# Performance work log

Hardware: AMD Instinct MI355X
Metric: run time of the kernel (lower is better)

## Reference

```python
import jax, jax.numpy as jnp
import numpy as np

NUM_BITS = 8
EPS = 1e-8
N_HEADS = 16

def fake_quantize(t):
    # per-tensor symmetric fake quantization, matching fake_quantize_tensor
    qmax = 2 ** (NUM_BITS - 1) - 1
    qmin = -(2 ** (NUM_BITS - 1))
    max_abs = jnp.max(jnp.abs(jax.lax.stop_gradient(t)))
    scale = jnp.maximum(max_abs / qmax, EPS)
    q = jnp.clip(jnp.round(t / scale), qmin, qmax)
    return q * scale

def fq_linear(x, W, b):
    # F.linear(fake_quant(x), fake_quant(W), b)
    return fake_quantize(x) @ fake_quantize(W).T + b

def setup_inputs() -> dict:
    key = jax.random.key(0)
    ks = jax.random.split(key, 9)
    B, T, D = 2, 2048, 1024
    s = 0.02
    return {
        "x": jax.random.normal(ks[0], (B, T, D), jnp.float32),
        "Wq": jax.random.normal(ks[1], (D, D), jnp.float32) * s,
        "bq": jax.random.normal(ks[2], (D,), jnp.float32) * s,
        "Wk": jax.random.normal(ks[3], (D, D), jnp.float32) * s,
        "bk": jax.random.normal(ks[4], (D,), jnp.float32) * s,
        "Wv": jax.random.normal(ks[5], (D, D), jnp.float32) * s,
        "bv": jax.random.normal(ks[6], (D,), jnp.float32) * s,
        "Wo": jax.random.normal(ks[7], (D, D), jnp.float32) * s,
        "bo": jax.random.normal(ks[8], (D,), jnp.float32) * s,
    }

def reference(x, Wq, bq, Wk, bk, Wv, bv, Wo, bo):
    B, T, D = x.shape
    H = N_HEADS
    Hd = D // H
    scale = Hd ** -0.5
    # projections (fake-quantized activations and weights)
    q = fq_linear(x, Wq, bq).reshape(B, T, H, Hd).transpose(0, 2, 1, 3)  # [B,H,T,Hd]
    k = fq_linear(x, Wk, bk).reshape(B, T, H, Hd).transpose(0, 2, 1, 3)
    v = fq_linear(x, Wv, bv).reshape(B, T, H, Hd).transpose(0, 2, 1, 3)
    # full T x T causal attention (faithful to the manual implementation)
    attn = jnp.einsum("bhqd,bhkd->bhqk", q, k) * scale  # [B,H,T,T]
    causal = jnp.tril(jnp.ones((T, T), dtype=bool))
    attn = jnp.where(causal, attn, -jnp.inf)
    attn = jax.nn.softmax(attn, axis=-1)  # dropout is identity at eval
    y = jnp.einsum("bhqk,bhkd->bhqd", attn, v)  # [B,H,T,Hd]
    y = y.transpose(0, 2, 1, 3).reshape(B, T, D)
    return fq_linear(y, Wo, bo)
```

## Files before the change

### kernel.cpp

```cpp
#include <hip/hip_runtime.h>
#include <hip/hip_fp16.h>

#define T_SEQ 2048
#define D_MODEL 1024
#define NB 2
#define NH 16
#define HD 64

using f16x8 = __attribute__((ext_vector_type(8))) _Float16;
using f16x4 = __attribute__((ext_vector_type(4))) _Float16;
using f32x4 = __attribute__((ext_vector_type(4))) float;
using i32x4 = __attribute__((ext_vector_type(4))) int;

#define ASLOT 32

__device__ __forceinline__ float fexp2(float x) { return __builtin_amdgcn_exp2f(x); }

__device__ __forceinline__ void gload_lds16(const void* g, void* l) {
    __builtin_amdgcn_global_load_lds((const __attribute__((address_space(1))) void*)g,
                                     (__attribute__((address_space(3))) void*)l, 16, 0, 0);
}

__global__ __launch_bounds__(256)
void k_absmax8(const float* __restrict__ x,
               const float* __restrict__ w0, const float* __restrict__ w1,
               const float* __restrict__ w2, const float* __restrict__ w3,
               unsigned int* __restrict__ amax) {
    __shared__ float wred[4];
    const int y = blockIdx.y;
    const float* p; int slot;
    if (y < 4) { p = x + (long)y * 1048576; slot = 0; }
    else { int w = y - 4; p = (w == 0) ? w0 : (w == 1) ? w1 : (w == 2) ? w2 : w3; slot = 1 + w; }
    const float4* p4 = (const float4*)p;
    const long i0 = (long)blockIdx.x * 256 + threadIdx.x;
    float m = 0.f;
    #pragma unroll 4
    for (int it = 0; it < 32; ++it) {
        float4 v = p4[i0 + (long)it * 8192];
        m = fmaxf(fmaxf(fmaxf(fabsf(v.x), fabsf(v.y)), fmaxf(fabsf(v.z), fabsf(v.w))), m);
    }
    #pragma unroll
    for (int off = 1; off < 64; off <<= 1) m = fmaxf(m, __shfl_xor(m, off));
    if ((threadIdx.x & 63) == 0) wred[threadIdx.x >> 6] = m;
    __syncthreads();
    if (threadIdx.x == 0) {
        float mm = fmaxf(fmaxf(wred[0], wred[1]), fmaxf(wred[2], wred[3]));
        if (mm > 0.f) atomicMax(amax + slot * ASLOT, __float_as_uint(mm));
    }
}

__device__ __forceinline__ unsigned int quant_pack4(float4 v, float scale) {
    int q0 = (int)fminf(127.f, fmaxf(-128.f, rintf(v.x / scale)));
    int q1 = (int)fminf(127.f, fmaxf(-128.f, rintf(v.y / scale)));
    int q2 = (int)fminf(127.f, fmaxf(-128.f, rintf(v.z / scale)));
    int q3 = (int)fminf(127.f, fmaxf(-128.f, rintf(v.w / scale)));
    return (q0 & 255) | ((q1 & 255) << 8) | ((q2 & 255) << 16) | ((q3 & 255) << 24);
}

__global__ __launch_bounds__(256)
void k_quant8(const float* __restrict__ x,
              const float* __restrict__ w0, const float* __restrict__ w1,
              const float* __restrict__ w2, const float* __restrict__ w3,
              char* __restrict__ xq,
              char* __restrict__ o0, char* __restrict__ o1,
              char* __restrict__ o2, char* __restrict__ o3,
              const unsigned int* __restrict__ amax) {
    const int y = blockIdx.y;
    const float* p; char* o; int slot;
    if (y < 4) { p = x + (long)y * 1048576; o = xq + (long)y * 1048576; slot = 0; }
    else {
        int w = y - 4;
        p = (w == 0) ? w0 : (w == 1) ? w1 : (w == 2) ? w2 : w3;
        o = (w == 0) ? o0 : (w == 1) ? o1 : (w == 2) ? o2 : o3;
        slot = 1 + w;
    }
    float scale = fmaxf(__uint_as_float(amax[slot * ASLOT]) / 127.0f, 1e-8f);
    const long n4 = 262144;
    long i = (long)blockIdx.x * blockDim.x + threadIdx.x;
    const long stride = (long)gridDim.x * blockDim.x;
    for (; i < n4; i += stride)
        ((unsigned int*)o)[i] = quant_pack4(((const float4*)p)[i], scale);
}

__global__ __launch_bounds__(256)
void k_quant_h(const _Float16* __restrict__ in, char* __restrict__ out,
               const unsigned int* __restrict__ amax, long n8) {
    float scale = fmaxf(__uint_as_float(*amax) / 127.0f, 1e-8f);
    long i = (long)blockIdx.x * blockDim.x + threadIdx.x;
    const long stride = (long)gridDim.x * blockDim.x;
    for (; i < n8; i += stride) {
        f16x8 v = ((const f16x8*)in)[i];
        unsigned int lo = 0, hi = 0;
        #pragma unroll
        for (int u = 0; u < 4; ++u) {
            int q = (int)fminf(127.f, fmaxf(-128.f, rintf((float)v[u] / scale)));
            lo |= (unsigned int)(q & 255) << (8 * u);
        }
        #pragma unroll
        for (int u = 0; u < 4; ++u) {
            int q = (int)fminf(127.f, fmaxf(-128.f, rintf((float)v[4 + u] / scale)));
            hi |= (unsigned int)(q & 255) << (8 * u);
        }
        ((uint2*)out)[i] = make_uint2(lo, hi);
    }
}

__device__ __forceinline__ void gemm_core8(const char* __restrict__ A,
                                           const char* __restrict__ Bw,
                                           int m0, int n0, int tid, i32x4 (&acc)[4][4]) {
    __shared__ char Asm[128 * 64];
    __shared__ char Bsm[128 * 64];
    const int lane = tid & 63, wid = tid >> 6;
    const int r16 = lane & 15, g = lane >> 4;
    const int wr = wid >> 1, wc = wid & 1;
    #pragma unroll
    for (int m = 0; m < 4; ++m)
        #pragma unroll
        for (int n = 0; n < 4; ++n) acc[m][n] = (i32x4){0, 0, 0, 0};
    for (int kt = 0; kt < 1024; kt += 64) {
        __syncthreads();
        #pragma unroll
        for (int s2 = 0; s2 < 2; ++s2) {
            int c = tid + s2 * 256;
            int row = c >> 2, cb = (c & 3) * 16;
            gload_lds16(&A[(long)(m0 + row) * 1024 + kt + cb], &Asm[c * 16]);
            gload_lds16(&Bw[(long)(n0 + row) * 1024 + kt + cb], &Bsm[c * 16]);
        }
        __syncthreads();
        i32x4 af[4], bf[4];
        #pragma unroll
        for (int m = 0; m < 4; ++m)
            af[m] = *(const i32x4*)&Asm[(wr * 64 + m * 16 + r16) * 64 + g * 16];
        #pragma unroll
        for (int n = 0; n < 4; ++n)
            bf[n] = *(const i32x4*)&Bsm[(wc * 64 + n * 16 + r16) * 64 + g * 16];
        #pragma unroll
        for (int m = 0; m < 4; ++m)
            #pragma unroll
            for (int n = 0; n < 4; ++n)
                acc[m][n] = __builtin_amdgcn_mfma_i32_16x16x64_i8(af[m], bf[n], acc[m][n], 0, 0, 0);
    }
}

__global__ __launch_bounds__(256)
void k_gemm_qkv(const char* __restrict__ A,
                const char* __restrict__ wq, const char* __restrict__ wk,
                const char* __restrict__ wv,
                const float* __restrict__ bq, const float* __restrict__ bk,
                const float* __restrict__ bv,
                const unsigned int* __restrict__ amax,
                _Float16* __restrict__ qo, _Float16* __restrict__ ko,
                _Float16* __restrict__ vto) {
    const int L = blockIdx.x;
    const int t = L >> 3;
    const int my = (L & 7) * 4 + (t & 3);
    const int nx = (t >> 2) & 7;
    const int z = t >> 5;
    const char* Bw = (z == 0) ? wq : (z == 1) ? wk : wv;
    const float* bias = (z == 0) ? bq : (z == 1) ? bk : bv;
    const int tid = threadIdx.x;
    const int m0 = my * 128, n0 = nx * 128;
    const int lane = tid & 63, wid = tid >> 6;
    const int r16 = lane & 15, g = lane >> 4;
    const int wr = wid >> 1, wc = wid & 1;

    i32x4 acc[4][4];
    gemm_core8(A, Bw, m0, n0, tid, acc);

    float sA = fmaxf(__uint_as_float(amax[0]) / 127.0f, 1e-8f);
    float sB = fmaxf(__uint_as_float(amax[(1 + z) * ASLOT]) / 127.0f, 1e-8f);
    float s = sA * sB;
    if (z < 2) {
        _Float16* out = (z == 0) ? qo : ko;
        #pragma unroll
        for (int m = 0; m < 4; ++m)
            #pragma unroll
            for (int n = 0; n < 4; ++n) {
                int col = n0 + wc * 64 + n * 16 + r16;
                float bcol = bias[col];
                int h = col >> 6, d = col & 63;
                #pragma unroll
                for (int r = 0; r < 4; ++r) {
                    int row = m0 + wr * 64 + m * 16 + g * 4 + r;
                    int b = row >> 11, tt = row & 2047;
                    out[(((long)(b * NH + h)) * T_SEQ + tt) * HD + d] =
                        (_Float16)((float)acc[m][n][r] * s + bcol);
                }
            }
    } else {
        #pragma unroll
        for (int m = 0; m < 4; ++m)
            #pragma unroll
            for (int n = 0; n < 4; ++n) {
                int col = n0 + wc * 64 + n * 16 + r16;
                float bcol = bias[col];
                int h = col >> 6, d = col & 63;
                int row0 = m0 + wr * 64 + m * 16 + g * 4;
                int b = row0 >> 11, tt = row0 & 2047;
                f16x4 pk;
                #pragma unroll
                for (int r = 0; r < 4; ++r) pk[r] = (_Float16)((float)acc[m][n][r] * s + bcol);
                *(f16x4*)&vto[(((long)(b * NH + h)) * HD + d) * T_SEQ + tt] = pk;
            }
    }
}

__global__ __launch_bounds__(256)
void k_gemm_o(const char* __restrict__ A, const char* __restrict__ Bw,
              const float* __restrict__ bias,
              const unsigned int* __restrict__ amaxA, const unsigned int* __restrict__ amaxB,
              float* __restrict__ out) {
    __shared__ char Asm[128 * 64];
    __shared__ char Bsm[64 * 64];
    const int L = blockIdx.x;
    const int t = L >> 3;
    const int my = (L & 7) * 4 + (t & 3);
    const int nx = t >> 2;
    const int tid = threadIdx.x;
    const int m0 = my * 128, n0 = nx * 64;
    const int lane = tid & 63, wid = tid >> 6;
    const int r16 = lane & 15, g = lane >> 4;
    const int wr = wid >> 1, wc = wid & 1;

    i32x4 acc[4][2];
    #pragma unroll
    for (int m = 0; m < 4; ++m)
        #pragma unroll
        for (int n = 0; n < 2; ++n) acc[m][n] = (i32x4){0, 0, 0, 0};

    for (int kt = 0; kt < 1024; kt += 64) {
        __syncthreads();
        #pragma unroll
        for (int s2 = 0; s2 < 2; ++s2) {
            int c = tid + s2 * 256;
            int row = c >> 2, cb = (c & 3) * 16;
            gload_lds16(&A[(long)(m0 + row) * 1024 + kt + cb], &Asm[c * 16]);
        }
        {
            int row = tid >> 2, cb = (tid & 3) * 16;
            gload_lds16(&Bw[(long)(n0 + row) * 1024 + kt + cb], &Bsm[tid * 16]);
        }
        __syncthreads();
        i32x4 af[4], bf[2];
        #pragma unroll
        for (int m = 0; m < 4; ++m)
            af[m] = *(const i32x4*)&Asm[(wr * 64 + m * 16 + r16) * 64 + g * 16];
        #pragma unroll
        for (int n = 0; n < 2; ++n)
            bf[n] = *(const i32x4*)&Bsm[(wc * 32 + n * 16 + r16) * 64 + g * 16];
        #pragma unroll
        for (int m = 0; m < 4; ++m)
            #pragma unroll
            for (int n = 0; n < 2; ++n)
                acc[m][n] = __builtin_amdgcn_mfma_i32_16x16x64_i8(af[m], bf[n], acc[m][n], 0, 0, 0);
    }

    float sA = fmaxf(__uint_as_float(*amaxA) / 127.0f, 1e-8f);
    float sB = fmaxf(__uint_as_float(*amaxB) / 127.0f, 1e-8f);
    float s = sA * sB;
    #pragma unroll
    for (int m = 0; m < 4; ++m)
        #pragma unroll
        for (int n = 0; n < 2; ++n) {
            int col = n0 + wc * 32 + n * 16 + r16;
            float bcol = bias[col];
            #pragma unroll
            for (int r = 0; r < 4; ++r) {
                int row = m0 + wr * 64 + m * 16 + g * 4 + r;
                out[(long)row * 1024 + col] = (float)acc[m][n][r] * s + bcol;
            }
        }
}

#define SOFTPV(S, MI)                                                                   \
    {                                                                                   \
        float t0_ = fmaxf(fmaxf(S[0][0], S[0][1]), fmaxf(S[0][2], S[0][3]));            \
        float t1_ = fmaxf(fmaxf(S[1][0], S[1][1]), fmaxf(S[1][2], S[1][3]));            \
        float t2_ = fmaxf(fmaxf(S[2][0], S[2][1]), fmaxf(S[2][2], S[2][3]));            \
        float t3_ = fmaxf(fmaxf(S[3][0], S[3][1]), fmaxf(S[3][2], S[3][3]));            \
        float Ml = fmaxf(fmaxf(t0_, t1_), fmaxf(t2_, t3_));                             \
        if (__any(Ml > mrun[MI] + 11.5f)) {                                             \
            float M = Ml;                                                               \
            _Pragma("unroll")                                                           \
            for (int off = 1; off < 64; off <<= 1) M = fmaxf(M, __shfl_xor(M, off));    \
            float corr = fexp2(mrun[MI] - M);                                           \
            _Pragma("unroll")                                                           \
            for (int r = 0; r < 4; ++r) lacc[MI][r] *= corr;                            \
            _Pragma("unroll")                                                           \
            for (int nb = 0; nb < 4; ++nb)                                              \
                _Pragma("unroll")                                                       \
                for (int r = 0; r < 4; ++r) oacc[MI][nb][r] *= corr;                    \
            mrun[MI] = M;                                                               \
        }                                                                               \
        _Pragma("unroll")                                                               \
        for (int nb = 0; nb < 4; ++nb)                                                  \
            _Pragma("unroll")                                                           \
            for (int r = 0; r < 4; ++r) {                                               \
                float pv = fexp2(S[nb][r] - mrun[MI]);                                  \
                lacc[MI][r] += pv;                                                      \
                int row = g * 4 + r, col = nb * 16 + r16;                               \
                int c8 = col >> 3;                                                      \
                Psm[wid][row * 64 + ((c8 ^ (row & 7)) << 3) + (col & 7)] = (_Float16)pv;\
            }                                                                           \
        f16x8 pa0 = *(const f16x8*)&Psm[wid][r16 * 64 + (((g)     ^ (r16 & 7)) << 3)];  \
        f16x8 pa1 = *(const f16x8*)&Psm[wid][r16 * 64 + (((4 + g) ^ (r16 & 7)) << 3)];  \
        __builtin_amdgcn_s_setprio(1);                                                  \
        _Pragma("unroll")                                                               \
        for (int nb = 0; nb < 4; ++nb) {                                                \
            int row = nb * 16 + r16;                                                    \
            f16x8 vb0 = *(const f16x8*)&Vc[row * 64 + (((g)     ^ (row & 7)) << 3)];    \
            f16x8 vb1 = *(const f16x8*)&Vc[row * 64 + (((4 + g) ^ (row & 7)) << 3)];    \
            oacc[MI][nb] = __builtin_amdgcn_mfma_f32_16x16x32_f16(pa0, vb0, oacc[MI][nb], 0, 0, 0); \
            oacc[MI][nb] = __builtin_amdgcn_mfma_f32_16x16x32_f16(pa1, vb1, oacc[MI][nb], 0, 0, 0); \
        }                                                                               \
        __builtin_amdgcn_s_setprio(0);                                                  \
    }

__global__ __launch_bounds__(256)
void k_attn(const _Float16* __restrict__ q, const _Float16* __restrict__ kk,
            const _Float16* __restrict__ vt,
            _Float16* __restrict__ Op, float2* __restrict__ ML) {
    __shared__ _Float16 Kd[2][4096];
    __shared__ _Float16 Vd[2][4096];
    __shared__ _Float16 Psm[4][1024];

    const int L = blockIdx.x;
    const int bh = (L & 7) * 4 + ((L >> 3) & 3);
    const int rest = L >> 5;
    const int p = rest >> 2, z = rest & 3;
    const int tid = threadIdx.x, wid = tid >> 6, lane = tid & 63;
    const int r16 = lane & 15, g = lane >> 4;
    const long base = (long)bh * T_SEQ * HD;
    const long vbase = (long)bh * HD * T_SEQ;
    const int nkh = 2 * (15 - p) + 2;
    const int a = (34 * z) >> 2, b2 = (34 * (z + 1)) >> 2;

    auto STAGE = [&](int jt, int buf) {
        const _Float16* kp = kk + base + (long)jt * 64 * HD;
        const _Float16* vp = vt + vbase + jt * 64;
        #pragma unroll
        for (int s2 = 0; s2 < 2; ++s2) {
            int slot = tid + s2 * 256;
            int row = slot >> 3;
            int ch = (slot & 7) ^ (row & 7);
            gload_lds16(kp + row * HD + ch * 8, &Kd[buf][slot * 8]);
            gload_lds16(vp + (long)row * T_SEQ + ch * 8, &Vd[buf][slot * 8]);
        }
    };

    #pragma unroll 1
    for (int sub = 0; sub < 2; ++sub) {
        const int J = sub ? p : (15 - p);
        const int nk = 2 * J + 2;
        const int lo = sub ? max(a - nkh, 0) : a;
        const int hi = sub ? max(b2 - nkh, 0) : min(b2, nk);
        const int t0 = J * 128;
        const long prow = (long)(z * 32 + bh) * T_SEQ + t0;

        if (lo >= hi) {
            f16x8 zz = {};
            #pragma unroll 1
            for (int i = tid; i < 1024; i += 256) {
                int row = i >> 3, ch = i & 7;
                *(f16x8*)&Op[(prow + row) * HD + ch * 8] = zz;
            }
            if (tid < 128) ML[prow + tid] = make_float2(-INFINITY, 0.f);
            continue;
        }

        f16x8 qf[2][2];
        #pragma unroll
        for (int m = 0; m < 2; ++m) {
            const _Float16* qp = q + base + (long)(t0 + m * 64 + wid * 16 + r16) * HD + g * 8;
            qf[m][0] = *(const f16x8*)qp;
            qf[m][1] = *(const f16x8*)(qp + 32);
            #pragma unroll
            for (int u = 0; u < 8; ++u) {
                qf[m][0][u] *= (_Float16)0.18033688f;
                qf[m][1][u] *= (_Float16)0.18033688f;
            }
        }
        float mrun[2] = {-INFINITY, -INFINITY};
        float lacc[2][4] = {{0.f, 0.f, 0.f, 0.f}, {0.f, 0.f, 0.f, 0.f}};
        f32x4 oacc[2][4];
        #pragma unroll
        for (int m = 0; m < 2; ++m)
            #pragma unroll
            for (int nb = 0; nb < 4; ++nb) oacc[m][nb] = (f32x4){0.f, 0.f, 0.f, 0.f};

        __syncthreads();
        STAGE(lo, 0);
        int cur = 0;
        for (int jt = lo; jt < hi; ++jt) {
            __syncthreads();
            if (jt + 1 < hi) STAGE(jt + 1, cur ^ 1);

            const _Float16* Kc = &Kd[cur][0];
            const _Float16* Vc = &Vd[cur][0];
            const bool skip0 = (jt == 2 * J + 1);

            f32x4 s0[4], s1[4];
            __builtin_amdgcn_s_setprio(1);
            #pragma unroll
            for (int nb = 0; nb < 4; ++nb) {
                int row = nb * 16 + r16;
                f16x8 kb0 = *(const f16x8*)&Kc[row * 64 + (((g)     ^ (row & 7)) << 3)];
                f16x8 kb1 = *(const f16x8*)&Kc[row * 64 + (((4 + g) ^ (row & 7)) << 3)];
                f32x4 a0 = (f32x4){0.f, 0.f, 0.f, 0.f};
                a0 = __builtin_amdgcn_mfma_f32_16x16x32_f16(qf[0][0], kb0, a0, 0, 0, 0);
                a0 = __builtin_amdgcn_mfma_f32_16x16x32_f16(qf[0][1], kb1, a0, 0, 0, 0);
                s0[nb] = a0;
                f32x4 a1 = (f32x4){0.f, 0.f, 0.f, 0.f};
                a1 = __builtin_amdgcn_mfma_f32_16x16x32_f16(qf[1][0], kb0, a1, 0, 0, 0);
                a1 = __builtin_amdgcn_mfma_f32_16x16x32_f16(qf[1][1], kb1, a1, 0, 0, 0);
                s1[nb] = a1;
            }
            __builtin_amdgcn_s_setprio(0);

            if (!skip0) {
                if (jt == 2 * J) {
                    #pragma unroll
                    for (int nb = 0; nb < 4; ++nb)
                        #pragma unroll
                        for (int r = 0; r < 4; ++r)
                            if (nb * 16 + r16 > wid * 16 + g * 4 + r) s0[nb][r] = -INFINITY;
                }
                SOFTPV(s0, 0)
            }
            if (jt == 2 * J + 1) {
                #pragma unroll
                for (int nb = 0; nb < 4; ++nb)
                    #pragma unroll
                    for (int r = 0; r < 4; ++r)
                        if (nb * 16 + r16 > wid * 16 + g * 4 + r) s1[nb][r] = -INFINITY;
            }
            SOFTPV(s1, 1)
            cur ^= 1;
        }
        #pragma unroll
        for (int m = 0; m < 2; ++m) {
            float lsum[4], linv[4];
            #pragma unroll
            for (int r = 0; r < 4; ++r) {
                float Lr = lacc[m][r];
                #pragma unroll
                for (int off = 1; off < 16; off <<= 1) Lr += __shfl_xor(Lr, off);
                lsum[r] = Lr;
                linv[r] = (Lr > 0.f) ? 1.f / Lr : 0.f;
            }
            #pragma unroll
            for (int nb = 0; nb < 4; ++nb)
                #pragma unroll
                for (int r = 0; r < 4; ++r)
                    Op[(prow + m * 64 + wid * 16 + g * 4 + r) * HD + nb * 16 + r16] =
                        (_Float16)(oacc[m][nb][r] * linv[r]);
            if (r16 == 0)
                #pragma unroll
                for (int r = 0; r < 4; ++r)
                    ML[prow + m * 64 + wid * 16 + g * 4 + r] =
                        make_float2(lsum[r] > 0.f ? mrun[m] : -INFINITY, lsum[r]);
        }
    }
}

__global__ __launch_bounds__(256)
void k_combine(const _Float16* __restrict__ Op, const float2* __restrict__ ML,
               _Float16* __restrict__ y, unsigned int* __restrict__ amax5) {
    __shared__ float wred[4];
    const int tid = threadIdx.x;
    const int c8 = (tid & 7) * 8;
    const int rsub = tid >> 3;
    float bmax = 0.f;
    #pragma unroll 1
    for (int it = 0; it < 8; ++it) {
        int row = blockIdx.x * 256 + it * 32 + rsub;
        float2 ml[4];
        #pragma unroll
        for (int zz = 0; zz < 4; ++zz) ml[zz] = ML[row + zz * 65536];
        float M = fmaxf(fmaxf(ml[0].x, ml[1].x), fmaxf(ml[2].x, ml[3].x));
        float w[4]; float den = 0.f;
        #pragma unroll
        for (int zz = 0; zz < 4; ++zz) { w[zz] = fexp2(ml[zz].x - M) * ml[zz].y; den += w[zz]; }
        float inv = 1.f / den;
        f16x8 o[4];
        #pragma unroll
        for (int zz = 0; zz < 4; ++zz)
            o[zz] = *(const f16x8*)&Op[(long)(row + zz * 65536) * HD + c8];
        f16x8 res;
        #pragma unroll
        for (int u = 0; u < 8; ++u) {
            float num = w[0] * (float)o[0][u] + w[1] * (float)o[1][u]
                      + w[2] * (float)o[2][u] + w[3] * (float)o[3][u];
            float val = num * inv;
            res[u] = (_Float16)val;
            bmax = fmaxf(bmax, fabsf(val));
        }
        int bh = row >> 11, t = row & 2047;
        *(f16x8*)&y[((long)((bh >> 4) * T_SEQ + t)) * D_MODEL + (bh & 15) * HD + c8] = res;
    }
    #pragma unroll
    for (int off = 1; off < 64; off <<= 1) bmax = fmaxf(bmax, __shfl_xor(bmax, off));
    if ((tid & 63) == 0) wred[tid >> 6] = bmax;
    __syncthreads();
    if (tid == 0) {
        float m = fmaxf(fmaxf(wred[0], wred[1]), fmaxf(wred[2], wred[3]));
        if (m > 0.f) atomicMax(amax5, __float_as_uint(m));
    }
}

extern "C" void kernel_launch(void* const* d_in, const int* in_sizes, int n_in,
                              void* d_out, int out_size, void* d_ws, size_t ws_size,
                              hipStream_t stream) {
    const float* x  = (const float*)d_in[0];
    const float* Wq = (const float*)d_in[1];
    const float* bq = (const float*)d_in[2];
    const float* Wk = (const float*)d_in[3];
    const float* bk = (const float*)d_in[4];
    const float* Wv = (const float*)d_in[5];
    const float* bv = (const float*)d_in[6];
    const float* Wo = (const float*)d_in[7];
    const float* bo = (const float*)d_in[8];

    char* ws = (char*)d_ws;
    unsigned int* amax = (unsigned int*)ws;
    char* xq8 = ws + 4096;
    char* wq8 = xq8 + 4194304L;
    char* wk8 = wq8 + 1048576L;
    char* wv8 = wk8 + 1048576L;
    char* wo8 = wv8 + 1048576L;
    char* p2 = ws + 4096 + 8388608L;
    _Float16* qh  = (_Float16*)p2;
    _Float16* kh  = (_Float16*)(p2 + 8388608L);
    _Float16* vth = (_Float16*)(p2 + 16777216L);
    _Float16* ybh = (_Float16*)(p2 + 25165824L);
    char*     yq8 = p2 + 33554432L;
    _Float16* Opart = (_Float16*)(p2 + 37748736L);
    float2*   MLp   = (float2*)(p2 + 71303168L);

    const long NY8 = (long)NB * T_SEQ * D_MODEL / 8;

    (void)hipMemsetAsync(amax, 0, 1024, stream);
    k_absmax8<<<dim3(32, 8), 256, 0, stream>>>(x, Wq, Wk, Wv, Wo, amax);
    k_quant8<<<dim3(128, 8), 256, 0, stream>>>(x, Wq, Wk, Wv, Wo,
                                               xq8, wq8, wk8, wv8, wo8, amax);
    k_gemm_qkv<<<768, 256, 0, stream>>>(xq8, wq8, wk8, wv8, bq, bk, bv,
                                        amax, qh, kh, vth);
    k_attn<<<1024, 256, 0, stream>>>(qh, kh, vth, Opart, MLp);
    k_combine<<<256, 256, 0, stream>>>(Opart, MLp, ybh, amax + 5 * ASLOT);
    k_quant_h<<<512, 256, 0, stream>>>(ybh, yq8, amax + 5 * ASLOT, NY8);
    k_gemm_o<<<512, 256, 0, stream>>>(yq8, wo8, bo, amax + 5 * ASLOT, amax + 4 * ASLOT,
                                      (float*)d_out);
}
```

Before: 126.7 us.

## Compute transposed S tile and redistribute P via bpermute instead of LDS

Swaps the MFMA operands so each lane holds scores for one query row across several keys. Row sums then reduce in-lane, and P is built as packed f16 registers that are shuffled into the A-operand layout with ds_bpermute, replacing the per-wave LDS round-trip through Psm. This removes the P shared-memory buffer, its scattered half-precision stores and the reload, and simplifies the final row-sum reduction. It also drops the s_setprio hints, and the bpermute traffic plus lane selects add cross-lane work in exchange.

```diff
diff --git a/kernel.cpp b/kernel.cpp
--- a/kernel.cpp
+++ b/kernel.cpp
@@ -9,8 +9,10 @@
 
 using f16x8 = __attribute__((ext_vector_type(8))) _Float16;
 using f16x4 = __attribute__((ext_vector_type(4))) _Float16;
+using f16x2 = __attribute__((ext_vector_type(2))) _Float16;
 using f32x4 = __attribute__((ext_vector_type(4))) float;
 using i32x4 = __attribute__((ext_vector_type(4))) int;
+using u32x4 = __attribute__((ext_vector_type(4))) unsigned int;
 
 #define ASLOT 32
 
@@ -284,27 +286,38 @@
             _Pragma("unroll")                                                           \
             for (int off = 1; off < 64; off <<= 1) M = fmaxf(M, __shfl_xor(M, off));    \
             float corr = fexp2(mrun[MI] - M);                                           \
-            _Pragma("unroll")                                                           \
-            for (int r = 0; r < 4; ++r) lacc[MI][r] *= corr;                            \
+            lacc[MI] *= corr;                                                           \
             _Pragma("unroll")                                                           \
             for (int nb = 0; nb < 4; ++nb)                                              \
                 _Pragma("unroll")                                                       \
                 for (int r = 0; r < 4; ++r) oacc[MI][nb][r] *= corr;                    \
             mrun[MI] = M;                                                               \
         }                                                                               \
+        unsigned int pk_[4][2];                                                         \
         _Pragma("unroll")                                                               \
-        for (int nb = 0; nb < 4; ++nb)                                                  \
+        for (int kb = 0; kb < 4; ++kb)                                                  \
             _Pragma("unroll")                                                           \
-            for (int r = 0; r < 4; ++r) {                                               \
-                float pv = fexp2(S[nb][r] - mrun[MI]);                                  \
-                lacc[MI][r] += pv;                                                      \
-                int row = g * 4 + r, col = nb * 16 + r16;                               \
-                int c8 = col >> 3;                                                      \
-                Psm[wid][row * 64 + ((c8 ^ (row & 7)) << 3) + (col & 7)] = (_Float16)pv;\
+            for (int j = 0; j < 2; ++j) {                                               \
+                float e0_ = fexp2(S[kb][2 * j]     - mrun[MI]);                         \
+                float e1_ = fexp2(S[kb][2 * j + 1] - mrun[MI]);                         \
+                lacc[MI] += e0_ + e1_;                                                  \
+                f16x2 h2_; h2_[0] = (_Float16)e0_; h2_[1] = (_Float16)e1_;              \
+                pk_[kb][j] = __builtin_bit_cast(unsigned int, h2_);                     \
             }                                                                           \
-        f16x8 pa0 = *(const f16x8*)&Psm[wid][r16 * 64 + (((g)     ^ (r16 & 7)) << 3)];  \
-        f16x8 pa1 = *(const f16x8*)&Psm[wid][r16 * 64 + (((4 + g) ^ (r16 & 7)) << 3)];  \
-        __builtin_amdgcn_s_setprio(1);                                                  \
+        u32x4 wa_, wb_;                                                                 \
+        _Pragma("unroll")                                                               \
+        for (int w = 0; w < 4; ++w) {                                                   \
+            int ad_ = (w < 2) ? alo_ : ahi_;                                            \
+            int jj_ = w & 1;                                                            \
+            int c0_ = __builtin_amdgcn_ds_bpermute(ad_, (int)pk_[0][jj_]);              \
+            int c1_ = __builtin_amdgcn_ds_bpermute(ad_, (int)pk_[1][jj_]);              \
+            int c2_ = __builtin_amdgcn_ds_bpermute(ad_, (int)pk_[2][jj_]);              \
+            int c3_ = __builtin_amdgcn_ds_bpermute(ad_, (int)pk_[3][jj_]);              \
+            wa_[w] = (unsigned int)(ghi_ ? c1_ : c0_);                                  \
+            wb_[w] = (unsigned int)(ghi_ ? c3_ : c2_);                                  \
+        }                                                                               \
+        f16x8 pa0 = __builtin_bit_cast(f16x8, wa_);                                     \
+        f16x8 pa1 = __builtin_bit_cast(f16x8, wb_);                                     \
         _Pragma("unroll")                                                               \
         for (int nb = 0; nb < 4; ++nb) {                                                \
             int row = nb * 16 + r16;                                                    \
@@ -313,7 +326,6 @@
             oacc[MI][nb] = __builtin_amdgcn_mfma_f32_16x16x32_f16(pa0, vb0, oacc[MI][nb], 0, 0, 0); \
             oacc[MI][nb] = __builtin_amdgcn_mfma_f32_16x16x32_f16(pa1, vb1, oacc[MI][nb], 0, 0, 0); \
         }                                                                               \
-        __builtin_amdgcn_s_setprio(0);                                                  \
     }
 
 __global__ __launch_bounds__(256)
@@ -322,7 +334,6 @@
             _Float16* __restrict__ Op, float2* __restrict__ ML) {
     __shared__ _Float16 Kd[2][4096];
     __shared__ _Float16 Vd[2][4096];
-    __shared__ _Float16 Psm[4][1024];
 
     const int L = blockIdx.x;
     const int bh = (L & 7) * 4 + ((L >> 3) & 3);
@@ -334,6 +345,9 @@
     const long vbase = (long)bh * HD * T_SEQ;
     const int nkh = 2 * (15 - p) + 2;
     const int a = (34 * z) >> 2, b2 = (34 * (z + 1)) >> 2;
+    const int alo_ = (r16 + ((g & 1) << 5)) << 2;
+    const int ahi_ = alo_ + 64;
+    const bool ghi_ = (g >= 2);
 
     auto STAGE = [&](int jt, int buf) {
         const _Float16* kp = kk + base + (long)jt * 64 * HD;
@@ -381,7 +395,7 @@
             }
         }
         float mrun[2] = {-INFINITY, -INFINITY};
-        float lacc[2][4] = {{0.f, 0.f, 0.f, 0.f}, {0.f, 0.f, 0.f, 0.f}};
+        float lacc[2] = {0.f, 0.f};
         f32x4 oacc[2][4];
         #pragma unroll
         for (int m = 0; m < 2; ++m)
@@ -400,65 +414,61 @@
             const bool skip0 = (jt == 2 * J + 1);
 
             f32x4 s0[4], s1[4];
-            __builtin_amdgcn_s_setprio(1);
             #pragma unroll
             for (int nb = 0; nb < 4; ++nb) {
                 int row = nb * 16 + r16;
                 f16x8 kb0 = *(const f16x8*)&Kc[row * 64 + (((g)     ^ (row & 7)) << 3)];
                 f16x8 kb1 = *(const f16x8*)&Kc[row * 64 + (((4 + g) ^ (row & 7)) << 3)];
                 f32x4 a0 = (f32x4){0.f, 0.f, 0.f, 0.f};
-                a0 = __builtin_amdgcn_mfma_f32_16x16x32_f16(qf[0][0], kb0, a0, 0, 0, 0);
-                a0 = __builtin_amdgcn_mfma_f32_16x16x32_f16(qf[0][1], kb1, a0, 0, 0, 0);
+                a0 = __builtin_amdgcn_mfma_f32_16x16x32_f16(kb0, qf[0][0], a0, 0, 0, 0);
+                a0 = __builtin_amdgcn_mfma_f32_16x16x32_f16(kb1, qf[0][1], a0, 0, 0, 0);
                 s0[nb] = a0;
                 f32x4 a1 = (f32x4){0.f, 0.f, 0.f, 0.f};
-                a1 = __builtin_amdgcn_mfma_f32_16x16x32_f16(qf[1][0], kb0, a1, 0, 0, 0);
-                a1 = __builtin_amdgcn_mfma_f32_16x16x32_f16(qf[1][1], kb1, a1, 0, 0, 0);
+                a1 = __builtin_amdgcn_mfma_f32_16x16x32_f16(kb0, qf[1][0], a1, 0, 0, 0);
+                a1 = __builtin_amdgcn_mfma_f32_16x16x32_f16(kb1, qf[1][1], a1, 0, 0, 0);
                 s1[nb] = a1;
             }
-            __builtin_amdgcn_s_setprio(0);
 
             if (!skip0) {
                 if (jt == 2 * J) {
                     #pragma unroll
-                    for (int nb = 0; nb < 4; ++nb)
+                    for (int kb = 0; kb < 4; ++kb)
                         #pragma unroll
                         for (int r = 0; r < 4; ++r)
-                            if (nb * 16 + r16 > wid * 16 + g * 4 + r) s0[nb][r] = -INFINITY;
+                            if (kb * 16 + g * 4 + r > wid * 16 + r16) s0[kb][r] = -INFINITY;
                 }
                 SOFTPV(s0, 0)
             }
             if (jt == 2 * J + 1) {
                 #pragma unroll
-                for (int nb = 0; nb < 4; ++nb)
+                for (int kb = 0; kb < 4; ++kb)
                     #pragma unroll
                     for (int r = 0; r < 4; ++r)
-                        if (nb * 16 + r16 > wid * 16 + g * 4 + r) s1[nb][r] = -INFINITY;
+                        if (kb * 16 + g * 4 + r > wid * 16 + r16) s1[kb][r] = -INFINITY;
             }
             SOFTPV(s1, 1)
             cur ^= 1;
         }
         #pragma unroll
         for (int m = 0; m < 2; ++m) {
-            float lsum[4], linv[4];
+            float l = lacc[m];
+            l += __shfl_xor(l, 16);
+            l += __shfl_xor(l, 32);
+            float linvr[4];
             #pragma unroll
             for (int r = 0; r < 4; ++r) {
-                float Lr = lacc[m][r];
-                #pragma unroll
-                for (int off = 1; off < 16; off <<= 1) Lr += __shfl_xor(Lr, off);
-                lsum[r] = Lr;
-                linv[r] = (Lr > 0.f) ? 1.f / Lr : 0.f;
+                float lr = __shfl(l, g * 4 + r);
+                linvr[r] = (lr > 0.f) ? 1.f / lr : 0.f;
             }
             #pragma unroll
             for (int nb = 0; nb < 4; ++nb)
                 #pragma unroll
                 for (int r = 0; r < 4; ++r)
                     Op[(prow + m * 64 + wid * 16 + g * 4 + r) * HD + nb * 16 + r16] =
-                        (_Float16)(oacc[m][nb][r] * linv[r]);
-            if (r16 == 0)
-                #pragma unroll
-                for (int r = 0; r < 4; ++r)
-                    ML[prow + m * 64 + wid * 16 + g * 4 + r] =
-                        make_float2(lsum[r] > 0.f ? mrun[m] : -INFINITY, lsum[r]);
+                        (_Float16)(oacc[m][nb][r] * linvr[r]);
+            if (lane < 16)
+                ML[prow + m * 64 + wid * 16 + r16] =
+                    make_float2(l > 0.f ? mrun[m] : -INFINITY, l);
         }
     }
 }
```

Measured after the change: 128.6 us. About the same (+1.5%).

## Double GEMM K-tile to 128 with XOR-swizzled LDS and interleave attention QK/PV

Applied to the files above, without the earlier changes.

The int8 QKV and output GEMMs now stage 128-wide K tiles instead of 64, which halves the number of barrier-separated load phases. An XOR swizzle on 16-byte chunks is applied to the LDS layout to avoid bank conflicts on the fragment reads. The attention inner loop is restructured so each of the two query sub-blocks computes its QK scores and then immediately runs softmax/PV, instead of computing both score sets first. This lowers register pressure and skips QK MFMAs for the masked sub-block, at the cost of doubling LDS use in the GEMMs, which may lower occupancy.

```diff
diff --git a/kernel.cpp b/kernel.cpp
--- a/kernel.cpp
+++ b/kernel.cpp
@@ -108,8 +108,8 @@
 __device__ __forceinline__ void gemm_core8(const char* __restrict__ A,
                                            const char* __restrict__ Bw,
                                            int m0, int n0, int tid, i32x4 (&acc)[4][4]) {
-    __shared__ char Asm[128 * 64];
-    __shared__ char Bsm[128 * 64];
+    __shared__ char Asm[128 * 128];
+    __shared__ char Bsm[128 * 128];
     const int lane = tid & 63, wid = tid >> 6;
     const int r16 = lane & 15, g = lane >> 4;
     const int wr = wid >> 1, wc = wid & 1;
@@ -117,28 +117,36 @@
     for (int m = 0; m < 4; ++m)
         #pragma unroll
         for (int n = 0; n < 4; ++n) acc[m][n] = (i32x4){0, 0, 0, 0};
-    for (int kt = 0; kt < 1024; kt += 64) {
+    for (int kt = 0; kt < 1024; kt += 128) {
         __syncthreads();
         #pragma unroll
-        for (int s2 = 0; s2 < 2; ++s2) {
+        for (int s2 = 0; s2 < 4; ++s2) {
             int c = tid + s2 * 256;
-            int row = c >> 2, cb = (c & 3) * 16;
-            gload_lds16(&A[(long)(m0 + row) * 1024 + kt + cb], &Asm[c * 16]);
-            gload_lds16(&Bw[(long)(n0 + row) * 1024 + kt + cb], &Bsm[c * 16]);
+            int row = c >> 3, ch = c & 7;
+            int chs = ch ^ (row & 7);
+            gload_lds16(&A[(long)(m0 + row) * 1024 + kt + chs * 16], &Asm[c * 16]);
+            gload_lds16(&Bw[(long)(n0 + row) * 1024 + kt + chs * 16], &Bsm[c * 16]);
         }
         __syncthreads();
-        i32x4 af[4], bf[4];
-        #pragma unroll
-        for (int m = 0; m < 4; ++m)
-            af[m] = *(const i32x4*)&Asm[(wr * 64 + m * 16 + r16) * 64 + g * 16];
-        #pragma unroll
-        for (int n = 0; n < 4; ++n)
-            bf[n] = *(const i32x4*)&Bsm[(wc * 64 + n * 16 + r16) * 64 + g * 16];
-        #pragma unroll
-        for (int m = 0; m < 4; ++m)
-            #pragma unroll
-            for (int n = 0; n < 4; ++n)
-                acc[m][n] = __builtin_amdgcn_mfma_i32_16x16x64_i8(af[m], bf[n], acc[m][n], 0, 0, 0);
+        #pragma unroll
+        for (int kk = 0; kk < 2; ++kk) {
+            i32x4 af[4], bf[4];
+            #pragma unroll
+            for (int m = 0; m < 4; ++m) {
+                int row = wr * 64 + m * 16 + r16;
+                af[m] = *(const i32x4*)&Asm[row * 128 + (((kk * 4 + g) ^ (row & 7)) << 4)];
+            }
+            #pragma unroll
+            for (int n = 0; n < 4; ++n) {
+                int row = wc * 64 + n * 16 + r16;
+                bf[n] = *(const i32x4*)&Bsm[row * 128 + (((kk * 4 + g) ^ (row & 7)) << 4)];
+            }
+            #pragma unroll
+            for (int m = 0; m < 4; ++m)
+                #pragma unroll
+                for (int n = 0; n < 4; ++n)
+                    acc[m][n] = __builtin_amdgcn_mfma_i32_16x16x64_i8(af[m], bf[n], acc[m][n], 0, 0, 0);
+        }
     }
 }
 
@@ -210,8 +218,8 @@
               const float* __restrict__ bias,
               const unsigned int* __restrict__ amaxA, const unsigned int* __restrict__ amaxB,
               float* __restrict__ out) {
-    __shared__ char Asm[128 * 64];
-    __shared__ char Bsm[64 * 64];
+    __shared__ char Asm[128 * 128];
+    __shared__ char Bsm[64 * 128];
     const int L = blockIdx.x;
     const int t = L >> 3;
     const int my = (L & 7) * 4 + (t & 3);
@@ -228,31 +236,42 @@
         #pragma unroll
         for (int n = 0; n < 2; ++n) acc[m][n] = (i32x4){0, 0, 0, 0};
 
-    for (int kt = 0; kt < 1024; kt += 64) {
+    for (int kt = 0; kt < 1024; kt += 128) {
         __syncthreads();
+        #pragma unroll
+        for (int s2 = 0; s2 < 4; ++s2) {
+            int c = tid + s2 * 256;
+            int row = c >> 3, ch = c & 7;
+            int chs = ch ^ (row & 7);
+            gload_lds16(&A[(long)(m0 + row) * 1024 + kt + chs * 16], &Asm[c * 16]);
+        }
         #pragma unroll
         for (int s2 = 0; s2 < 2; ++s2) {
             int c = tid + s2 * 256;
-            int row = c >> 2, cb = (c & 3) * 16;
-            gload_lds16(&A[(long)(m0 + row) * 1024 + kt + cb], &Asm[c * 16]);
-        }
-        {
-            int row = tid >> 2, cb = (tid & 3) * 16;
-            gload_lds16(&Bw[(long)(n0 + row) * 1024 + kt + cb], &Bsm[tid * 16]);
+            int row = c >> 3, ch = c & 7;
+            int chs = ch ^ (row & 7);
+            gload_lds16(&Bw[(long)(n0 + row) * 1024 + kt + chs * 16], &Bsm[c * 16]);
         }
         __syncthreads();
-        i32x4 af[4], bf[2];
-        #pragma unroll
-        for (int m = 0; m < 4; ++m)
-            af[m] = *(const i32x4*)&Asm[(wr * 64 + m * 16 + r16) * 64 + g * 16];
-        #pragma unroll
-        for (int n = 0; n < 2; ++n)
-            bf[n] = *(const i32x4*)&Bsm[(wc * 32 + n * 16 + r16) * 64 + g * 16];
-        #pragma unroll
-        for (int m = 0; m < 4; ++m)
-            #pragma unroll
-            for (int n = 0; n < 2; ++n)
-                acc[m][n] = __builtin_amdgcn_mfma_i32_16x16x64_i8(af[m], bf[n], acc[m][n], 0, 0, 0);
+        #pragma unroll
+        for (int kk = 0; kk < 2; ++kk) {
+            i32x4 af[4], bf[2];
+            #pragma unroll
+            for (int m = 0; m < 4; ++m) {
+                int row = wr * 64 + m * 16 + r16;
+                af[m] = *(const i32x4*)&Asm[row * 128 + (((kk * 4 + g) ^ (row & 7)) << 4)];
+            }
+            #pragma unroll
+            for (int n = 0; n < 2; ++n) {
+                int row = wc * 32 + n * 16 + r16;
+                bf[n] = *(const i32x4*)&Bsm[row * 128 + (((kk * 4 + g) ^ (row & 7)) << 4)];
+            }
+            #pragma unroll
+            for (int m = 0; m < 4; ++m)
+                #pragma unroll
+                for (int n = 0; n < 2; ++n)
+                    acc[m][n] = __builtin_amdgcn_mfma_i32_16x16x64_i8(af[m], bf[n], acc[m][n], 0, 0, 0);
+        }
     }
 
     float sA = fmaxf(__uint_as_float(*amaxA) / 127.0f, 1e-8f);
@@ -398,43 +417,31 @@
             const _Float16* Kc = &Kd[cur][0];
             const _Float16* Vc = &Vd[cur][0];
             const bool skip0 = (jt == 2 * J + 1);
-
-            f32x4 s0[4], s1[4];
-            __builtin_amdgcn_s_setprio(1);
-            #pragma unroll
-            for (int nb = 0; nb < 4; ++nb) {
-                int row = nb * 16 + r16;
-                f16x8 kb0 = *(const f16x8*)&Kc[row * 64 + (((g)     ^ (row & 7)) << 3)];
-                f16x8 kb1 = *(const f16x8*)&Kc[row * 64 + (((4 + g) ^ (row & 7)) << 3)];
-                f32x4 a0 = (f32x4){0.f, 0.f, 0.f, 0.f};
-                a0 = __builtin_amdgcn_mfma_f32_16x16x32_f16(qf[0][0], kb0, a0, 0, 0, 0);
-                a0 = __builtin_amdgcn_mfma_f32_16x16x32_f16(qf[0][1], kb1, a0, 0, 0, 0);
-                s0[nb] = a0;
-                f32x4 a1 = (f32x4){0.f, 0.f, 0.f, 0.f};
-                a1 = __builtin_amdgcn_mfma_f32_16x16x32_f16(qf[1][0], kb0, a1, 0, 0, 0);
-                a1 = __builtin_amdgcn_mfma_f32_16x16x32_f16(qf[1][1], kb1, a1, 0, 0, 0);
-                s1[nb] = a1;
-            }
-            __builtin_amdgcn_s_setprio(0);
-
-            if (!skip0) {
-                if (jt == 2 * J) {
+            #pragma unroll
+            for (int m = 0; m < 2; ++m) {
+                if (m == 0 && skip0) continue;
+                f32x4 s[4];
+                __builtin_amdgcn_s_setprio(1);
+                #pragma unroll
+                for (int nb = 0; nb < 4; ++nb) {
+                    int row = nb * 16 + r16;
+                    f16x8 kb0 = *(const f16x8*)&Kc[row * 64 + (((g)     ^ (row & 7)) << 3)];
+                    f16x8 kb1 = *(const f16x8*)&Kc[row * 64 + (((4 + g) ^ (row & 7)) << 3)];
+                    f32x4 a0 = (f32x4){0.f, 0.f, 0.f, 0.f};
+                    a0 = __builtin_amdgcn_mfma_f32_16x16x32_f16(qf[m][0], kb0, a0, 0, 0, 0);
+                    a0 = __builtin_amdgcn_mfma_f32_16x16x32_f16(qf[m][1], kb1, a0, 0, 0, 0);
+                    s[nb] = a0;
+                }
+                __builtin_amdgcn_s_setprio(0);
+                if (jt == 2 * J + m) {
                     #pragma unroll
                     for (int nb = 0; nb < 4; ++nb)
                         #pragma unroll
                         for (int r = 0; r < 4; ++r)
-                            if (nb * 16 + r16 > wid * 16 + g * 4 + r) s0[nb][r] = -INFINITY;
+                            if (nb * 16 + r16 > wid * 16 + g * 4 + r) s[nb][r] = -INFINITY;
                 }
-                SOFTPV(s0, 0)
-            }
-            if (jt == 2 * J + 1) {
-                #pragma unroll
-                for (int nb = 0; nb < 4; ++nb)
-                    #pragma unroll
-                    for (int r = 0; r < 4; ++r)
-                        if (nb * 16 + r16 > wid * 16 + g * 4 + r) s1[nb][r] = -INFINITY;
-            }
-            SOFTPV(s1, 1)
+                SOFTPV(s, m)
+            }
             cur ^= 1;
         }
         #pragma unroll
```

After: 123.4 us. -2.6%, faster.
